# Performance work log

Hardware: AMD Instinct MI355X
Metric: run time of the kernel (lower is better)

The kernel has to match this reference:

```python
import jax, jax.numpy as jnp
import numpy as np

DIM, HEADS, DIM_HEAD, DY_DIM = 256, 8, 64, 16
INNER = HEADS * DIM_HEAD
B, N = 4, 1024
EPS = 1e-5


def _leaky(x):
    return jnp.where(x >= 0, x, 0.01 * x)


def _gelu(x):
    return jax.nn.gelu(x, approximate=False)  # torch nn.GELU default (erf)


def setup_inputs() -> dict:
    key = jax.random.key(0)
    ks = jax.random.split(key, 14)

    def lin(k, fan_in, fan_out):
        bound = 1.0 / np.sqrt(fan_in)
        return jax.random.uniform(k, (fan_in, fan_out), jnp.float32, -bound, bound)

    return {
        "xyzs": jax.random.normal(ks[0], (B, N, 3), jnp.float32),
        "features": jax.random.normal(ks[1], (B, N, DIM), jnp.float32),
        "gamma": jnp.ones((DIM,), jnp.float32),
        "beta": jnp.zeros((DIM,), jnp.float32),
        "W_qkv": lin(ks[2], DIM, 3 * INNER),
        "W_pos1": lin(ks[3], 3, DY_DIM),
        "W_pos2": lin(ks[4], DY_DIM, 3),
        "W_neg1": lin(ks[5], 3, DY_DIM),
        "W_neg2": lin(ks[6], DY_DIM, 3),
        "W_cross": lin(ks[7], 3, 3),
        "b_cross": jax.random.uniform(ks[8], (3,), jnp.float32, -0.5, 0.5),
        "W_spatial": lin(ks[9], 3, DIM_HEAD),
        "W_out": lin(ks[10], INNER, DIM),
        "b_out": jax.random.uniform(ks[11], (DIM,), jnp.float32, -1.0 / np.sqrt(INNER), 1.0 / np.sqrt(INNER)),
    }


def reference(xyzs, features, gamma, beta, W_qkv, W_pos1, W_pos2, W_neg1, W_neg2,
              W_cross, b_cross, W_spatial, W_out, b_out):
    b, n, dim = features.shape
    d = W_spatial.shape[1]                       # dim_head
    h = W_qkv.shape[1] // (3 * d)                # heads
    scale = d ** -0.5

    # LayerNorm
    mu = jnp.mean(features, axis=-1, keepdims=True)
    var = jnp.var(features, axis=-1, keepdims=True)
    x = (features - mu) * jax.lax.rsqrt(var + EPS) * gamma + beta

    # qkv projection -> (b, h, n, d)
    qkv = x @ W_qkv                              # (b, n, 3*h*d)
    q, k, v = jnp.split(qkv, 3, axis=-1)
    to_bhnd = lambda t: t.reshape(b, n, h, d).transpose(0, 2, 1, 3)
    q, k, v = to_bhnd(q), to_bhnd(k), to_bhnd(v)

    # pairwise deltas: delta[b, i, j] = xyzs[b, j] - xyzs[b, i]  (b, n, n, 3)
    delta = xyzs[:, None, :, :] - xyzs[:, :, None, :]

    pos = _leaky(_gelu(jax.nn.relu(delta) @ W_pos1) @ W_pos2)
    neg = _leaky(_gelu(jax.nn.relu(-delta) @ W_neg1) @ W_neg2)
    cross = _leaky((pos * neg) @ W_cross + b_cross)
    delta = cross * delta                        # (b, n, n, 3)

    # full softmax attention
    dots = jnp.einsum('bhid,bhjd->bhij', q, k) * scale
    attn = jax.nn.softmax(dots, axis=-1)         # (b, h, n, n)

    v_out = jnp.einsum('bhij,bhjd->bhid', attn, v)
    # attention-weighted reduction of pairwise deltas (no (b,h,n,n,3) materialization)
    wdelta = jnp.einsum('bhij,bijc->bhic', attn, delta)   # (b, h, n, 3)
    disp = wdelta @ W_spatial                    # (b, h, n, d)

    out = (v_out + disp).transpose(0, 2, 1, 3).reshape(b, n, h * d)
    out = _gelu(out @ W_out + b_out)             # to_out: Linear + GELU (dropout=0)
    return out + features
```

## Files before the change

### kernel.cpp

```cpp
#include <hip/hip_runtime.h>
#include <hip/hip_bf16.h>
#include <math.h>

#define BB 4
#define NN 1024
#define DIMM 256
#define HEADS 8
#define DH 64
#define INNERD 512
#define NT 16
#define MDPLANE 4194304

typedef __bf16 bf16x8 __attribute__((ext_vector_type(8)));
typedef float f32x4 __attribute__((ext_vector_type(4)));
typedef _Float16 h2 __attribute__((ext_vector_type(2)));

__device__ __forceinline__ h2 h2s(float v) {
    _Float16 h = (_Float16)v;
    h2 r; r.x = h; r.y = h;
    return r;
}

__device__ __forceinline__ float gelu_poly(float x) {
    float xc = fminf(fmaxf(x, -3.0f), 3.0f);
    float u = xc * xc;
    float f = fmaf(u, fmaf(u, fmaf(u, fmaf(u, 4.4413e-5f, -1.33195e-3f),
                                   1.70980e-2f), -1.299964e-1f), 7.9734583e-1f);
    float E = xc * f;
    float hx = 0.5f * xc;
    float g = fmaf(hx, E, hx);
    return g + fmaxf(x - 3.0f, 0.0f);
}

__device__ __forceinline__ h2 gelu_h2(h2 x) {
    h2 xc = __builtin_elementwise_min(__builtin_elementwise_max(x, h2s(-3.0f)), h2s(3.0f));
    h2 u = xc * xc;
    h2 f = u * h2s(2.22065e-5f) + h2s(-6.65975e-4f);
    f = u * f + h2s(8.549e-3f);
    f = u * f + h2s(-6.49982e-2f);
    f = u * f + h2s(0.39867292f);
    h2 g = xc * h2s(0.5f) + u * f;
    h2 tail = __builtin_elementwise_max(x - h2s(3.0f), h2s(0.0f));
    return g + tail;
}
__device__ __forceinline__ h2 leaky_h2(h2 x) {
    return __builtin_elementwise_max(x, x * h2s(0.01f));
}

__global__ __launch_bounds__(256) void prep_kernel(const float* __restrict__ feat,
                                                   const float* __restrict__ gamma,
                                                   const float* __restrict__ beta,
                                                   __hip_bfloat16* __restrict__ xb,
                                                   const float* __restrict__ Wqkv,
                                                   __hip_bfloat16* __restrict__ Wt,
                                                   const float* __restrict__ Wout,
                                                   __hip_bfloat16* __restrict__ Wot,
                                                   const float* __restrict__ Wp1,
                                                   const float* __restrict__ Wp2,
                                                   const float* __restrict__ Wn1,
                                                   const float* __restrict__ Wn2,
                                                   const float* __restrict__ Wc,
                                                   const float* __restrict__ bc,
                                                   unsigned int* __restrict__ wh) {
    __shared__ float smem[64 * 65];
    int bx = blockIdx.x;
    int tid = threadIdx.x;
    if (bx < 4096) {
        int row = bx;
        float v = feat[row * DIMM + tid];
        float s = v, ss = v * v;
        #pragma unroll
        for (int off = 1; off < 64; off <<= 1) {
            s += __shfl_xor(s, off);
            ss += __shfl_xor(ss, off);
        }
        float* red = smem;
        int w = tid >> 6, lane = tid & 63;
        if (lane == 0) { red[w] = s; red[4 + w] = ss; }
        __syncthreads();
        s = red[0] + red[1] + red[2] + red[3];
        ss = red[4] + red[5] + red[6] + red[7];
        float mu = s * (1.0f / DIMM);
        float var = ss * (1.0f / DIMM) - mu * mu;
        float rs = rsqrtf(var + 1e-5f);
        xb[row * DIMM + tid] = __float2bfloat16((v - mu) * rs * gamma[tid] + beta[tid]);
    } else if (bx < 4224) {
        const float* W;
        __hip_bfloat16* Wd;
        int C, R, nx, ky;
        if (bx < 4192) {
            int t = bx - 4096;
            W = Wqkv; Wd = Wt; C = 1536; R = 256;
            nx = t % 24; ky = t / 24;
        } else {
            int t = bx - 4192;
            W = Wout; Wd = Wot; C = 256; R = 512;
            nx = t % 4; ky = t / 4;
        }
        int n0 = nx * 64, k0 = ky * 64;
        int cc = tid & 63, rr = tid >> 6;
        #pragma unroll
        for (int p = 0; p < 16; ++p) {
            int k = rr + p * 4;
            smem[k * 65 + cc] = W[(k0 + k) * C + n0 + cc];
        }
        __syncthreads();
        #pragma unroll
        for (int p = 0; p < 16; ++p) {
            int n = rr + p * 4;
            Wd[(n0 + n) * R + k0 + cc] = __float2bfloat16(smem[cc * 65 + n]);
        }
    } else {
        int t = tid;
        if (t < 204) {
            float v;
            if (t < 48) v = Wp1[t];
            else if (t < 96) v = Wp2[t - 48];
            else if (t < 144) v = Wn1[t - 96];
            else if (t < 192) v = Wn2[t - 144];
            else if (t < 201) v = Wc[t - 192];
            else v = bc[t - 201];
            _Float16 h = (_Float16)v;
            unsigned short us = __builtin_bit_cast(unsigned short, h);
            wh[t] = (unsigned int)us | ((unsigned int)us << 16);
        }
    }
}

__device__ __forceinline__ void qkv_body(int bx,
                                         const __hip_bfloat16* __restrict__ xb,
                                         const __hip_bfloat16* __restrict__ Wt,
                                         __hip_bfloat16* __restrict__ qb,
                                         __hip_bfloat16* __restrict__ kb,
                                         __hip_bfloat16* __restrict__ vtb) {
    int mt = bx & 63, nt = bx >> 6;
    int tid = threadIdx.x, w = tid >> 6, lane = tid & 63;
    int g = lane >> 4, c = lane & 15;

    const __hip_bfloat16* ap = xb + (mt * 64 + w * 16 + c) * 256 + g * 8;
    bf16x8 a[8];
    #pragma unroll
    for (int ks = 0; ks < 8; ++ks) a[ks] = *reinterpret_cast<const bf16x8*>(ap + ks * 32);

    f32x4 acc[4];
    #pragma unroll
    for (int jf = 0; jf < 4; ++jf) { acc[jf][0] = 0.f; acc[jf][1] = 0.f; acc[jf][2] = 0.f; acc[jf][3] = 0.f; }

    const __hip_bfloat16* bp = Wt + (nt * 64 + c) * 256 + g * 8;
    #pragma unroll
    for (int jf = 0; jf < 4; ++jf) {
        const __hip_bfloat16* bpj = bp + jf * 16 * 256;
        #pragma unroll
        for (int ks = 0; ks < 8; ++ks) {
            bf16x8 bfrag = *reinterpret_cast<const bf16x8*>(bpj + ks * 32);
            acc[jf] = __builtin_amdgcn_mfma_f32_16x16x32_bf16(a[ks], bfrag, acc[jf], 0, 0, 0);
        }
    }

    int col0 = nt * 64;
    int part = col0 >> 9;
    int h = (col0 >> 6) & 7;
    #pragma unroll
    for (int jf = 0; jf < 4; ++jf) {
        int d = jf * 16 + c;
        #pragma unroll
        for (int r = 0; r < 4; ++r) {
            int m = mt * 64 + w * 16 + g * 4 + r;
            int b = m >> 10, nn = m & 1023;
            if (part == 0)
                qb[(((b * HEADS + h) * NN) + nn) * DH + d] = __float2bfloat16(acc[jf][r] * 0.125f);
            else if (part == 1)
                kb[(((b * HEADS + h) * NN) + nn) * DH + d] = __float2bfloat16(acc[jf][r]);
            else
                vtb[((long)(b * HEADS + h) * DH + d) * NN + nn] = __float2bfloat16(acc[jf][r]);
        }
    }
}

__device__ __forceinline__ void dmlp_body(int bx,
                                          const float* __restrict__ xyz,
                                          const unsigned int* __restrict__ wlds_u,
                                          _Float16* __restrict__ md) {
    int tid = threadIdx.x;
    int bi0 = bx * 4;
    int b = bi0 >> 10;
    const float* xj = xyz + (long)b * NN * 3;

    float xia[4], xib[4], xic[4];
    #pragma unroll
    for (int rr = 0; rr < 4; ++rr) {
        xia[rr] = xyz[(bi0 + rr) * 3 + 0];
        xib[rr] = xyz[(bi0 + rr) * 3 + 1];
        xic[rr] = xyz[(bi0 + rr) * 3 + 2];
    }

    const h2* w = (const h2*)wlds_u;

    h2 d0[8], d1[8], d2[8];
    #pragma unroll
    for (int g = 0; g < 2; ++g) {
        int j = 2 * tid + g * 512;
        const float* pj = xj + j * 3;
        float e0 = pj[0], e1 = pj[1], e2 = pj[2];
        float f0 = pj[3], f1 = pj[4], f2 = pj[5];
        #pragma unroll
        for (int rr = 0; rr < 4; ++rr) {
            int cg = rr * 2 + g;
            d0[cg].x = (_Float16)(e0 - xia[rr]); d0[cg].y = (_Float16)(f0 - xia[rr]);
            d1[cg].x = (_Float16)(e1 - xib[rr]); d1[cg].y = (_Float16)(f1 - xib[rr]);
            d2[cg].x = (_Float16)(e2 - xic[rr]); d2[cg].y = (_Float16)(f2 - xic[rr]);
        }
    }

    h2 pp0[8], pp1[8], pp2[8], nv0[8], nv1[8], nv2[8];
    {
        h2 r0[8], r1[8], r2[8], a0[8], a1[8], a2[8];
        #pragma unroll
        for (int cg = 0; cg < 8; ++cg) {
            r0[cg] = __builtin_elementwise_max(d0[cg], h2s(0.f));
            r1[cg] = __builtin_elementwise_max(d1[cg], h2s(0.f));
            r2[cg] = __builtin_elementwise_max(d2[cg], h2s(0.f));
            a0[cg] = h2s(0.f); a1[cg] = h2s(0.f); a2[cg] = h2s(0.f);
        }
        #pragma unroll
        for (int m = 0; m < 16; ++m) {
            h2 w0 = w[m], w1 = w[16 + m], w2 = w[32 + m];
            h2 u0 = w[48 + 3 * m], u1 = w[48 + 3 * m + 1], u2 = w[48 + 3 * m + 2];
            #pragma unroll
            for (int cg = 0; cg < 8; ++cg) {
                h2 t = r0[cg] * w0 + r1[cg] * w1 + r2[cg] * w2;
                t = gelu_h2(t);
                a0[cg] = a0[cg] + t * u0;
                a1[cg] = a1[cg] + t * u1;
                a2[cg] = a2[cg] + t * u2;
            }
        }
        #pragma unroll
        for (int cg = 0; cg < 8; ++cg) {
            pp0[cg] = leaky_h2(a0[cg]); pp1[cg] = leaky_h2(a1[cg]); pp2[cg] = leaky_h2(a2[cg]);
        }
    }
    {
        h2 r0[8], r1[8], r2[8], a0[8], a1[8], a2[8];
        #pragma unroll
        for (int cg = 0; cg < 8; ++cg) {
            r0[cg] = __builtin_elementwise_max(h2s(0.f) - d0[cg], h2s(0.f));
            r1[cg] = __builtin_elementwise_max(h2s(0.f) - d1[cg], h2s(0.f));
            r2[cg] = __builtin_elementwise_max(h2s(0.f) - d2[cg], h2s(0.f));
            a0[cg] = h2s(0.f); a1[cg] = h2s(0.f); a2[cg] = h2s(0.f);
        }
        #pragma unroll
        for (int m = 0; m < 16; ++m) {
            h2 w0 = w[96 + m], w1 = w[96 + 16 + m], w2 = w[96 + 32 + m];
            h2 u0 = w[144 + 3 * m], u1 = w[144 + 3 * m + 1], u2 = w[144 + 3 * m + 2];
            #pragma unroll
            for (int cg = 0; cg < 8; ++cg) {
                h2 t = r0[cg] * w0 + r1[cg] * w1 + r2[cg] * w2;
                t = gelu_h2(t);
                a0[cg] = a0[cg] + t * u0;
                a1[cg] = a1[cg] + t * u1;
                a2[cg] = a2[cg] + t * u2;
            }
        }
        #pragma unroll
        for (int cg = 0; cg < 8; ++cg) {
            nv0[cg] = leaky_h2(a0[cg]); nv1[cg] = leaky_h2(a1[cg]); nv2[cg] = leaky_h2(a2[cg]);
        }
    }

    h2 c00 = w[192], c01 = w[193], c02 = w[194];
    h2 c10 = w[195], c11 = w[196], c12 = w[197];
    h2 c20 = w[198], c21 = w[199], c22 = w[200];
    h2 b0 = w[201], b1 = w[202], b2 = w[203];

    unsigned int* st0 = (unsigned int*)md;
    unsigned int* st1 = (unsigned int*)(md + MDPLANE);
    unsigned int* st2 = (unsigned int*)(md + 2 * MDPLANE);
    #pragma unroll
    for (int rr = 0; rr < 4; ++rr) {
        long dwbase = (long)(bi0 + rr) * 512;
        #pragma unroll
        for (int g = 0; g < 2; ++g) {
            int cg = rr * 2 + g;
            h2 q0 = pp0[cg] * nv0[cg], q1 = pp1[cg] * nv1[cg], q2 = pp2[cg] * nv2[cg];
            h2 c0 = leaky_h2(q0 * c00 + q1 * c10 + q2 * c20 + b0);
            h2 c1 = leaky_h2(q0 * c01 + q1 * c11 + q2 * c21 + b1);
            h2 c2 = leaky_h2(q0 * c02 + q1 * c12 + q2 * c22 + b2);
            h2 m0 = c0 * d0[cg], m1 = c1 * d1[cg], m2 = c2 * d2[cg];
            long idx = dwbase + tid + g * 256;
            st0[idx] = __builtin_bit_cast(unsigned int, m0);
            st1[idx] = __builtin_bit_cast(unsigned int, m1);
            st2[idx] = __builtin_bit_cast(unsigned int, m2);
        }
    }
}

__global__ __launch_bounds__(256, 4) void fused_mid(const float* __restrict__ xyz,
                                                    const unsigned int* __restrict__ wh,
                                                    _Float16* __restrict__ md,
                                                    const __hip_bfloat16* __restrict__ xb,
                                                    const __hip_bfloat16* __restrict__ Wt,
                                                    __hip_bfloat16* __restrict__ qb,
                                                    __hip_bfloat16* __restrict__ kb,
                                                    __hip_bfloat16* __restrict__ vtb) {
    __shared__ unsigned int wlds[204];
    int bx = blockIdx.x;
    if (bx < 1024) {
        if (threadIdx.x < 204) wlds[threadIdx.x] = wh[threadIdx.x];
        __syncthreads();
        dmlp_body(bx, xyz, wlds, md);
    } else {
        qkv_body(bx - 1024, xb, Wt, qb, kb, vtb);
    }
}

__global__ __launch_bounds__(256) void attn_kernel(
    const __hip_bfloat16* __restrict__ q,
    const __hip_bfloat16* __restrict__ kk,
    const __hip_bfloat16* __restrict__ vt,
    const _Float16* __restrict__ md,
    const float* __restrict__ Wsp,
    __hip_bfloat16* __restrict__ yb)
{
    int it = blockIdx.x, h = blockIdx.y, b = blockIdx.z;
    int tid = threadIdx.x;
    int w = tid >> 6, lane = tid & 63;
    int g = lane >> 4, c = lane & 15;

    __shared__ __align__(16) __hip_bfloat16 k_lds[2][64][64];
    __shared__ __align__(16) __hip_bfloat16 v_lds[2][64][64];
    __shared__ __align__(16) __hip_bfloat16 p_lds[4][16][64];

    const __hip_bfloat16* qp = q + ((long)(b * HEADS + h) * NN + it * 64) * DH;
    const __hip_bfloat16* kp = kk + (long)(b * HEADS + h) * NN * DH;
    const __hip_bfloat16* vp = vt + (long)(b * HEADS + h) * DH * NN;

    bf16x8 qa[2];
    #pragma unroll
    for (int t2 = 0; t2 < 2; ++t2)
        qa[t2] = *reinterpret_cast<const bf16x8*>(qp + (w * 16 + c) * DH + t2 * 32 + g * 8);

    int r0 = tid >> 3;
    int d00 = (tid & 7) * 8;
    int4 kreg[2], vreg[2];

    f32x4 o[4];
    #pragma unroll
    for (int df = 0; df < 4; ++df) { o[df][0] = 0.f; o[df][1] = 0.f; o[df][2] = 0.f; o[df][3] = 0.f; }
    float m_[4] = {-1e30f, -1e30f, -1e30f, -1e30f};
    float l_[4] = {0.f, 0.f, 0.f, 0.f};
    float wdx[4] = {0.f, 0.f, 0.f, 0.f}, wdy[4] = {0.f, 0.f, 0.f, 0.f}, wdz[4] = {0.f, 0.f, 0.f, 0.f};

    #pragma unroll
    for (int c2 = 0; c2 < 2; ++c2) {
        int r = r0 + c2 * 32;
        kreg[c2] = *reinterpret_cast<const int4*>(kp + (0 * 64 + r) * DH + d00);
        vreg[c2] = *reinterpret_cast<const int4*>(vp + (long)r * NN + 0 * 64 + d00);
    }
    #pragma unroll
    for (int c2 = 0; c2 < 2; ++c2) {
        int r = r0 + c2 * 32;
        int sd = d00 ^ ((r & 7) << 3);
        *reinterpret_cast<int4*>(&k_lds[0][r][sd]) = kreg[c2];
        *reinterpret_cast<int4*>(&v_lds[0][r][sd]) = vreg[c2];
    }
    __syncthreads();

    const _Float16* md0 = md;
    const _Float16* md1 = md + MDPLANE;
    const _Float16* md2 = md + 2 * MDPLANE;
    long mdrow = (long)(b * NN + it * 64 + w * 16 + g * 4) * NN + c;

    for (int t = 0; t < NT; ++t) {
        int buf = t & 1;
        if (t + 1 < NT) {
            #pragma unroll
            for (int c2 = 0; c2 < 2; ++c2) {
                int r = r0 + c2 * 32;
                kreg[c2] = *reinterpret_cast<const int4*>(kp + ((t + 1) * 64 + r) * DH + d00);
                vreg[c2] = *reinterpret_cast<const int4*>(vp + (long)r * NN + (t + 1) * 64 + d00);
            }
        }

        float mdc[4][4][3];
        #pragma unroll
        for (int r = 0; r < 4; ++r) {
            long off = mdrow + (long)r * NN + t * 64;
            #pragma unroll
            for (int jf = 0; jf < 4; ++jf) {
                mdc[r][jf][0] = (float)md0[off + jf * 16];
                mdc[r][jf][1] = (float)md1[off + jf * 16];
                mdc[r][jf][2] = (float)md2[off + jf * 16];
            }
        }

        f32x4 s[4];
        #pragma unroll
        for (int jf = 0; jf < 4; ++jf) {
            f32x4 acc = {0.f, 0.f, 0.f, 0.f};
            int jl = jf * 16 + c;
            int sw = (jl & 7) << 3;
            #pragma unroll
            for (int t2 = 0; t2 < 2; ++t2) {
                bf16x8 bk = *reinterpret_cast<const bf16x8*>(&k_lds[buf][jl][(t2 * 32 + g * 8) ^ sw]);
                acc = __builtin_amdgcn_mfma_f32_16x16x32_bf16(qa[t2], bk, acc, 0, 0, 0);
            }
            s[jf] = acc;
        }

        float pe[4][4];
        #pragma unroll
        for (int r = 0; r < 4; ++r) {
            float tm = fmaxf(fmaxf(s[0][r], s[1][r]), fmaxf(s[2][r], s[3][r]));
            tm = fmaxf(tm, __shfl_xor(tm, 1));
            tm = fmaxf(tm, __shfl_xor(tm, 2));
            tm = fmaxf(tm, __shfl_xor(tm, 4));
            tm = fmaxf(tm, __shfl_xor(tm, 8));
            float nm = fmaxf(m_[r], tm);
            float corr = __expf(m_[r] - nm);
            m_[r] = nm;
            l_[r] *= corr;
            wdx[r] *= corr; wdy[r] *= corr; wdz[r] *= corr;
            o[0][r] *= corr; o[1][r] *= corr; o[2][r] *= corr; o[3][r] *= corr;
            float ps = 0.f;
            #pragma unroll
            for (int jf = 0; jf < 4; ++jf) {
                float p = __expf(s[jf][r] - nm);
                pe[r][jf] = p;
                ps += p;
            }
            l_[r] += ps;
        }

        #pragma unroll
        for (int r = 0; r < 4; ++r) {
            int row = g * 4 + r;
            int sw = (row & 7) << 3;
            #pragma unroll
            for (int jf = 0; jf < 4; ++jf)
                p_lds[w][row][(jf * 16 + c) ^ sw] = __float2bfloat16(pe[r][jf]);
        }
        asm volatile("s_waitcnt lgkmcnt(0)" ::: "memory");

        #pragma unroll
        for (int r = 0; r < 4; ++r) {
            #pragma unroll
            for (int jf = 0; jf < 4; ++jf) {
                wdx[r] = fmaf(pe[r][jf], mdc[r][jf][0], wdx[r]);
                wdy[r] = fmaf(pe[r][jf], mdc[r][jf][1], wdy[r]);
                wdz[r] = fmaf(pe[r][jf], mdc[r][jf][2], wdz[r]);
            }
        }

        #pragma unroll
        for (int t2 = 0; t2 < 2; ++t2) {
            int swp = (c & 7) << 3;
            bf16x8 pa = *reinterpret_cast<const bf16x8*>(&p_lds[w][c][(t2 * 32 + g * 8) ^ swp]);
            #pragma unroll
            for (int df = 0; df < 4; ++df) {
                int dl = df * 16 + c;
                int swv = (dl & 7) << 3;
                bf16x8 bv = *reinterpret_cast<const bf16x8*>(&v_lds[buf][dl][(t2 * 32 + g * 8) ^ swv]);
                o[df] = __builtin_amdgcn_mfma_f32_16x16x32_bf16(pa, bv, o[df], 0, 0, 0);
            }
        }

        if (t + 1 < NT) {
            #pragma unroll
            for (int c2 = 0; c2 < 2; ++c2) {
                int r = r0 + c2 * 32;
                int sd = d00 ^ ((r & 7) << 3);
                *reinterpret_cast<int4*>(&k_lds[buf ^ 1][r][sd]) = kreg[c2];
                *reinterpret_cast<int4*>(&v_lds[buf ^ 1][r][sd]) = vreg[c2];
            }
        }
        __syncthreads();
    }

    #pragma unroll
    for (int r = 0; r < 4; ++r) {
        float lv = l_[r];
        lv += __shfl_xor(lv, 1); lv += __shfl_xor(lv, 2);
        lv += __shfl_xor(lv, 4); lv += __shfl_xor(lv, 8);
        float w0 = wdx[r], w1 = wdy[r], w2 = wdz[r];
        w0 += __shfl_xor(w0, 1); w0 += __shfl_xor(w0, 2); w0 += __shfl_xor(w0, 4); w0 += __shfl_xor(w0, 8);
        w1 += __shfl_xor(w1, 1); w1 += __shfl_xor(w1, 2); w1 += __shfl_xor(w1, 4); w1 += __shfl_xor(w1, 8);
        w2 += __shfl_xor(w2, 1); w2 += __shfl_xor(w2, 2); w2 += __shfl_xor(w2, 4); w2 += __shfl_xor(w2, 8);
        float inv = 1.0f / lv;
        w0 *= inv; w1 *= inv; w2 *= inv;
        int row = g * 4 + r;
        long ig = (long)b * NN + it * 64 + w * 16 + row;
        __hip_bfloat16* yp = yb + ig * INNERD + h * DH;
        #pragma unroll
        for (int df = 0; df < 4; ++df) {
            int d = df * 16 + c;
            float disp = w0 * Wsp[d] + w1 * Wsp[64 + d] + w2 * Wsp[128 + d];
            yp[d] = __float2bfloat16(o[df][r] * inv + disp);
        }
    }
}

__global__ __launch_bounds__(256) void out_gemm(const __hip_bfloat16* __restrict__ yb,
                                                const __hip_bfloat16* __restrict__ Wot,
                                                const float* __restrict__ bout,
                                                const float* __restrict__ feat,
                                                float* __restrict__ out) {
    int mt = blockIdx.x, nt = blockIdx.y;
    int tid = threadIdx.x, w = tid >> 6, lane = tid & 63;
    int g = lane >> 4, c = lane & 15;

    const __hip_bfloat16* ap = yb + ((long)mt * 64 + w * 16 + c) * INNERD + g * 8;
    bf16x8 a[16];
    #pragma unroll
    for (int ks = 0; ks < 16; ++ks) a[ks] = *reinterpret_cast<const bf16x8*>(ap + ks * 32);

    f32x4 acc[4];
    #pragma unroll
    for (int jf = 0; jf < 4; ++jf) { acc[jf][0] = 0.f; acc[jf][1] = 0.f; acc[jf][2] = 0.f; acc[jf][3] = 0.f; }

    const __hip_bfloat16* bp = Wot + (nt * 64 + c) * INNERD + g * 8;
    #pragma unroll
    for (int jf = 0; jf < 4; ++jf) {
        const __hip_bfloat16* bpj = bp + jf * 16 * INNERD;
        #pragma unroll
        for (int ks = 0; ks < 16; ++ks) {
            bf16x8 bfrag = *reinterpret_cast<const bf16x8*>(bpj + ks * 32);
            acc[jf] = __builtin_amdgcn_mfma_f32_16x16x32_bf16(a[ks], bfrag, acc[jf], 0, 0, 0);
        }
    }

    #pragma unroll
    for (int jf = 0; jf < 4; ++jf) {
        int d = nt * 64 + jf * 16 + c;
        float bo = bout[d];
        #pragma unroll
        for (int r = 0; r < 4; ++r) {
            long m = (long)mt * 64 + w * 16 + g * 4 + r;
            float val = gelu_poly(acc[jf][r] + bo);
            out[m * DIMM + d] = val + feat[m * DIMM + d];
        }
    }
}

extern "C" void kernel_launch(void* const* d_in, const int* in_sizes, int n_in,
                              void* d_out, int out_size, void* d_ws, size_t ws_size,
                              hipStream_t stream) {
    const float* xyzs  = (const float*)d_in[0];
    const float* feat  = (const float*)d_in[1];
    const float* gamma = (const float*)d_in[2];
    const float* beta  = (const float*)d_in[3];
    const float* Wqkv  = (const float*)d_in[4];
    const float* Wp1   = (const float*)d_in[5];
    const float* Wp2   = (const float*)d_in[6];
    const float* Wn1   = (const float*)d_in[7];
    const float* Wn2   = (const float*)d_in[8];
    const float* Wc    = (const float*)d_in[9];
    const float* bc    = (const float*)d_in[10];
    const float* Wsp   = (const float*)d_in[11];
    const float* Wout  = (const float*)d_in[12];
    const float* bout  = (const float*)d_in[13];
    float* out = (float*)d_out;

    __hip_bfloat16* xb  = (__hip_bfloat16*)d_ws;
    __hip_bfloat16* Wt  = xb + 1048576;
    __hip_bfloat16* Wot = Wt + 393216;
    __hip_bfloat16* qb  = Wot + 131072;
    __hip_bfloat16* kb  = qb + 2097152;
    __hip_bfloat16* vtb = kb + 2097152;
    __hip_bfloat16* yb  = vtb + 2097152;
    _Float16* md = (_Float16*)(yb + 2097152);
    unsigned int* wh = (unsigned int*)(md + 3 * MDPLANE);

    prep_kernel<<<4225, 256, 0, stream>>>(feat, gamma, beta, xb, Wqkv, Wt, Wout, Wot,
                                          Wp1, Wp2, Wn1, Wn2, Wc, bc, wh);
    fused_mid<<<2560, 256, 0, stream>>>(xyzs, wh, md, xb, Wt, qb, kb, vtb);
    attn_kernel<<<dim3(16, HEADS, BB), 256, 0, stream>>>(qb, kb, vtb, md, Wsp, yb);
    out_gemm<<<dim3(64, 4), 256, 0, stream>>>(yb, Wot, bout, feat, out);
}
```

Baseline: 118.9 us.

## Split attention key range in two with a separate combine kernel

The attention grid doubles so each block processes half of the key tiles. Each block writes unnormalized partial outputs, its running max, its softmax sum and its weighted-delta sums to an fp32 workspace. A new combine kernel rescales and merges the two halves, applies the spatial projection and writes the bf16 activations. This raises the number of blocks available to fill the GPU, at the cost of extra global traffic for the partials and one more kernel launch.

```diff
diff --git a/kernel.cpp b/kernel.cpp
--- a/kernel.cpp
+++ b/kernel.cpp
@@ -10,6 +10,7 @@
 #define INNERD 512
 #define NT 16
 #define MDPLANE 4194304
+#define TOTROWS 32768
 
 typedef __bf16 bf16x8 __attribute__((ext_vector_type(8)));
 typedef float f32x4 __attribute__((ext_vector_type(4)));
@@ -319,10 +320,12 @@
     const __hip_bfloat16* __restrict__ kk,
     const __hip_bfloat16* __restrict__ vt,
     const _Float16* __restrict__ md,
-    const float* __restrict__ Wsp,
-    __hip_bfloat16* __restrict__ yb)
+    float* __restrict__ po,
+    float* __restrict__ pml)
 {
-    int it = blockIdx.x, h = blockIdx.y, b = blockIdx.z;
+    int it = blockIdx.x, h = blockIdx.y;
+    int z = blockIdx.z;
+    int b = z & 3, jh = z >> 2;
     int tid = threadIdx.x;
     int w = tid >> 6, lane = tid & 63;
     int g = lane >> 4, c = lane & 15;
@@ -351,11 +354,12 @@
     float l_[4] = {0.f, 0.f, 0.f, 0.f};
     float wdx[4] = {0.f, 0.f, 0.f, 0.f}, wdy[4] = {0.f, 0.f, 0.f, 0.f}, wdz[4] = {0.f, 0.f, 0.f, 0.f};
 
+    int t0 = jh * 8;
     #pragma unroll
     for (int c2 = 0; c2 < 2; ++c2) {
         int r = r0 + c2 * 32;
-        kreg[c2] = *reinterpret_cast<const int4*>(kp + (0 * 64 + r) * DH + d00);
-        vreg[c2] = *reinterpret_cast<const int4*>(vp + (long)r * NN + 0 * 64 + d00);
+        kreg[c2] = *reinterpret_cast<const int4*>(kp + (t0 * 64 + r) * DH + d00);
+        vreg[c2] = *reinterpret_cast<const int4*>(vp + (long)r * NN + t0 * 64 + d00);
     }
     #pragma unroll
     for (int c2 = 0; c2 < 2; ++c2) {
@@ -371,21 +375,22 @@
     const _Float16* md2 = md + 2 * MDPLANE;
     long mdrow = (long)(b * NN + it * 64 + w * 16 + g * 4) * NN + c;
 
-    for (int t = 0; t < NT; ++t) {
+    for (int t = 0; t < 8; ++t) {
+        int tt = t0 + t;
         int buf = t & 1;
-        if (t + 1 < NT) {
+        if (t + 1 < 8) {
             #pragma unroll
             for (int c2 = 0; c2 < 2; ++c2) {
                 int r = r0 + c2 * 32;
-                kreg[c2] = *reinterpret_cast<const int4*>(kp + ((t + 1) * 64 + r) * DH + d00);
-                vreg[c2] = *reinterpret_cast<const int4*>(vp + (long)r * NN + (t + 1) * 64 + d00);
+                kreg[c2] = *reinterpret_cast<const int4*>(kp + ((tt + 1) * 64 + r) * DH + d00);
+                vreg[c2] = *reinterpret_cast<const int4*>(vp + (long)r * NN + (tt + 1) * 64 + d00);
             }
         }
 
         float mdc[4][4][3];
         #pragma unroll
         for (int r = 0; r < 4; ++r) {
-            long off = mdrow + (long)r * NN + t * 64;
+            long off = mdrow + (long)r * NN + tt * 64;
             #pragma unroll
             for (int jf = 0; jf < 4; ++jf) {
                 mdc[r][jf][0] = (float)md0[off + jf * 16];
@@ -465,7 +470,7 @@
             }
         }
 
-        if (t + 1 < NT) {
+        if (t + 1 < 8) {
             #pragma unroll
             for (int c2 = 0; c2 < 2; ++c2) {
                 int r = r0 + c2 * 32;
@@ -486,18 +491,42 @@
         w0 += __shfl_xor(w0, 1); w0 += __shfl_xor(w0, 2); w0 += __shfl_xor(w0, 4); w0 += __shfl_xor(w0, 8);
         w1 += __shfl_xor(w1, 1); w1 += __shfl_xor(w1, 2); w1 += __shfl_xor(w1, 4); w1 += __shfl_xor(w1, 8);
         w2 += __shfl_xor(w2, 1); w2 += __shfl_xor(w2, 2); w2 += __shfl_xor(w2, 4); w2 += __shfl_xor(w2, 8);
-        float inv = 1.0f / lv;
-        w0 *= inv; w1 *= inv; w2 *= inv;
-        int row = g * 4 + r;
-        long ig = (long)b * NN + it * 64 + w * 16 + row;
-        __hip_bfloat16* yp = yb + ig * INNERD + h * DH;
-        #pragma unroll
-        for (int df = 0; df < 4; ++df) {
-            int d = df * 16 + c;
-            float disp = w0 * Wsp[d] + w1 * Wsp[64 + d] + w2 * Wsp[128 + d];
-            yp[d] = __float2bfloat16(o[df][r] * inv + disp);
-        }
-    }
+        int row = w * 16 + g * 4 + r;
+        long grow = (long)(b * HEADS + h) * NN + it * 64 + row;
+        float* pop = po + ((long)jh * TOTROWS + grow) * 64;
+        #pragma unroll
+        for (int df = 0; df < 4; ++df)
+            pop[df * 16 + c] = o[df][r];
+        if (c == 0) {
+            float* pm = pml + ((long)jh * TOTROWS + grow) * 8;
+            pm[0] = m_[r]; pm[1] = lv; pm[2] = w0; pm[3] = w1; pm[4] = w2;
+        }
+    }
+}
+
+__global__ __launch_bounds__(256) void combine_kernel(const float* __restrict__ po,
+                                                      const float* __restrict__ pml,
+                                                      const float* __restrict__ Wsp,
+                                                      __hip_bfloat16* __restrict__ yb) {
+    long row = (long)blockIdx.x * 4 + (threadIdx.x >> 6);
+    int d = threadIdx.x & 63;
+    const float* pm0 = pml + row * 8;
+    const float* pm1 = pml + ((long)TOTROWS + row) * 8;
+    float m0 = pm0[0], l0 = pm0[1];
+    float m1 = pm1[0], l1 = pm1[1];
+    float m = fmaxf(m0, m1);
+    float a0 = __expf(m0 - m), a1 = __expf(m1 - m);
+    float l = fmaf(l0, a0, l1 * a1);
+    float inv = 1.0f / l;
+    float ov = fmaf(po[row * 64 + d], a0, po[((long)TOTROWS + row) * 64 + d] * a1) * inv;
+    float wd0 = fmaf(pm0[2], a0, pm1[2] * a1) * inv;
+    float wd1 = fmaf(pm0[3], a0, pm1[3] * a1) * inv;
+    float wd2 = fmaf(pm0[4], a0, pm1[4] * a1) * inv;
+    float disp = wd0 * Wsp[d] + wd1 * Wsp[64 + d] + wd2 * Wsp[128 + d];
+    int b = (int)(row >> 13);
+    int h = (int)((row >> 10) & 7);
+    int i = (int)(row & 1023);
+    yb[((long)(b * NN + i)) * INNERD + h * DH + d] = __float2bfloat16(ov + disp);
 }
 
 __global__ __launch_bounds__(256) void out_gemm(const __hip_bfloat16* __restrict__ yb,
@@ -570,10 +599,13 @@
     __hip_bfloat16* yb  = vtb + 2097152;
     _Float16* md = (_Float16*)(yb + 2097152);
     unsigned int* wh = (unsigned int*)(md + 3 * MDPLANE);
+    float* po  = (float*)(wh + 256);
+    float* pml = po + 2L * TOTROWS * 64;
 
     prep_kernel<<<4225, 256, 0, stream>>>(feat, gamma, beta, xb, Wqkv, Wt, Wout, Wot,
                                           Wp1, Wp2, Wn1, Wn2, Wc, bc, wh);
     fused_mid<<<2560, 256, 0, stream>>>(xyzs, wh, md, xb, Wt, qb, kb, vtb);
-    attn_kernel<<<dim3(16, HEADS, BB), 256, 0, stream>>>(qb, kb, vtb, md, Wsp, yb);
+    attn_kernel<<<dim3(16, HEADS, BB * 2), 256, 0, stream>>>(qb, kb, vtb, md, po, pml);
+    combine_kernel<<<TOTROWS / 4, 256, 0, stream>>>(po, pml, Wsp, yb);
     out_gemm<<<dim3(64, 4), 256, 0, stream>>>(yb, Wot, bout, feat, out);
 }
```

Result: slower. 127.2 us (+6.9%).

## Regroup delta MLP with layernorm prep and split QKV GEMM into own kernel

Applied to the files above, without the earlier changes.

Moves the pairwise delta MLP work out of the QKV-GEMM kernel and into the first kernel alongside layernorm and weight transposes, converting the small MLP weights to fp16 in each block's shared memory instead of through a workspace buffer. The QKV GEMM becomes a standalone launch. The aim is to overlap the independent delta MLP with prep work rather than with the GEMM, and to drop the packed-weight round trip. It changes which work shares the GPU at once, which may help or hurt load balance.

```diff
diff --git a/kernel.cpp b/kernel.cpp
--- a/kernel.cpp
+++ b/kernel.cpp
@@ -45,136 +45,6 @@
 }
 __device__ __forceinline__ h2 leaky_h2(h2 x) {
     return __builtin_elementwise_max(x, x * h2s(0.01f));
-}
-
-__global__ __launch_bounds__(256) void prep_kernel(const float* __restrict__ feat,
-                                                   const float* __restrict__ gamma,
-                                                   const float* __restrict__ beta,
-                                                   __hip_bfloat16* __restrict__ xb,
-                                                   const float* __restrict__ Wqkv,
-                                                   __hip_bfloat16* __restrict__ Wt,
-                                                   const float* __restrict__ Wout,
-                                                   __hip_bfloat16* __restrict__ Wot,
-                                                   const float* __restrict__ Wp1,
-                                                   const float* __restrict__ Wp2,
-                                                   const float* __restrict__ Wn1,
-                                                   const float* __restrict__ Wn2,
-                                                   const float* __restrict__ Wc,
-                                                   const float* __restrict__ bc,
-                                                   unsigned int* __restrict__ wh) {
-    __shared__ float smem[64 * 65];
-    int bx = blockIdx.x;
-    int tid = threadIdx.x;
-    if (bx < 4096) {
-        int row = bx;
-        float v = feat[row * DIMM + tid];
-        float s = v, ss = v * v;
-        #pragma unroll
-        for (int off = 1; off < 64; off <<= 1) {
-            s += __shfl_xor(s, off);
-            ss += __shfl_xor(ss, off);
-        }
-        float* red = smem;
-        int w = tid >> 6, lane = tid & 63;
-        if (lane == 0) { red[w] = s; red[4 + w] = ss; }
-        __syncthreads();
-        s = red[0] + red[1] + red[2] + red[3];
-        ss = red[4] + red[5] + red[6] + red[7];
-        float mu = s * (1.0f / DIMM);
-        float var = ss * (1.0f / DIMM) - mu * mu;
-        float rs = rsqrtf(var + 1e-5f);
-        xb[row * DIMM + tid] = __float2bfloat16((v - mu) * rs * gamma[tid] + beta[tid]);
-    } else if (bx < 4224) {
-        const float* W;
-        __hip_bfloat16* Wd;
-        int C, R, nx, ky;
-        if (bx < 4192) {
-            int t = bx - 4096;
-            W = Wqkv; Wd = Wt; C = 1536; R = 256;
-            nx = t % 24; ky = t / 24;
-        } else {
-            int t = bx - 4192;
-            W = Wout; Wd = Wot; C = 256; R = 512;
-            nx = t % 4; ky = t / 4;
-        }
-        int n0 = nx * 64, k0 = ky * 64;
-        int cc = tid & 63, rr = tid >> 6;
-        #pragma unroll
-        for (int p = 0; p < 16; ++p) {
-            int k = rr + p * 4;
-            smem[k * 65 + cc] = W[(k0 + k) * C + n0 + cc];
-        }
-        __syncthreads();
-        #pragma unroll
-        for (int p = 0; p < 16; ++p) {
-            int n = rr + p * 4;
-            Wd[(n0 + n) * R + k0 + cc] = __float2bfloat16(smem[cc * 65 + n]);
-        }
-    } else {
-        int t = tid;
-        if (t < 204) {
-            float v;
-            if (t < 48) v = Wp1[t];
-            else if (t < 96) v = Wp2[t - 48];
-            else if (t < 144) v = Wn1[t - 96];
-            else if (t < 192) v = Wn2[t - 144];
-            else if (t < 201) v = Wc[t - 192];
-            else v = bc[t - 201];
-            _Float16 h = (_Float16)v;
-            unsigned short us = __builtin_bit_cast(unsigned short, h);
-            wh[t] = (unsigned int)us | ((unsigned int)us << 16);
-        }
-    }
-}
-
-__device__ __forceinline__ void qkv_body(int bx,
-                                         const __hip_bfloat16* __restrict__ xb,
-                                         const __hip_bfloat16* __restrict__ Wt,
-                                         __hip_bfloat16* __restrict__ qb,
-                                         __hip_bfloat16* __restrict__ kb,
-                                         __hip_bfloat16* __restrict__ vtb) {
-    int mt = bx & 63, nt = bx >> 6;
-    int tid = threadIdx.x, w = tid >> 6, lane = tid & 63;
-    int g = lane >> 4, c = lane & 15;
-
-    const __hip_bfloat16* ap = xb + (mt * 64 + w * 16 + c) * 256 + g * 8;
-    bf16x8 a[8];
-    #pragma unroll
-    for (int ks = 0; ks < 8; ++ks) a[ks] = *reinterpret_cast<const bf16x8*>(ap + ks * 32);
-
-    f32x4 acc[4];
-    #pragma unroll
-    for (int jf = 0; jf < 4; ++jf) { acc[jf][0] = 0.f; acc[jf][1] = 0.f; acc[jf][2] = 0.f; acc[jf][3] = 0.f; }
-
-    const __hip_bfloat16* bp = Wt + (nt * 64 + c) * 256 + g * 8;
-    #pragma unroll
-    for (int jf = 0; jf < 4; ++jf) {
-        const __hip_bfloat16* bpj = bp + jf * 16 * 256;
-        #pragma unroll
-        for (int ks = 0; ks < 8; ++ks) {
-            bf16x8 bfrag = *reinterpret_cast<const bf16x8*>(bpj + ks * 32);
-            acc[jf] = __builtin_amdgcn_mfma_f32_16x16x32_bf16(a[ks], bfrag, acc[jf], 0, 0, 0);
-        }
-    }
-
-    int col0 = nt * 64;
-    int part = col0 >> 9;
-    int h = (col0 >> 6) & 7;
-    #pragma unroll
-    for (int jf = 0; jf < 4; ++jf) {
-        int d = jf * 16 + c;
-        #pragma unroll
-        for (int r = 0; r < 4; ++r) {
-            int m = mt * 64 + w * 16 + g * 4 + r;
-            int b = m >> 10, nn = m & 1023;
-            if (part == 0)
-                qb[(((b * HEADS + h) * NN) + nn) * DH + d] = __float2bfloat16(acc[jf][r] * 0.125f);
-            else if (part == 1)
-                kb[(((b * HEADS + h) * NN) + nn) * DH + d] = __float2bfloat16(acc[jf][r]);
-            else
-                vtb[((long)(b * HEADS + h) * DH + d) * NN + nn] = __float2bfloat16(acc[jf][r]);
-        }
-    }
 }
 
 __device__ __forceinline__ void dmlp_body(int bx,
@@ -295,22 +165,136 @@
     }
 }
 
-__global__ __launch_bounds__(256, 4) void fused_mid(const float* __restrict__ xyz,
-                                                    const unsigned int* __restrict__ wh,
-                                                    _Float16* __restrict__ md,
-                                                    const __hip_bfloat16* __restrict__ xb,
-                                                    const __hip_bfloat16* __restrict__ Wt,
-                                                    __hip_bfloat16* __restrict__ qb,
-                                                    __hip_bfloat16* __restrict__ kb,
-                                                    __hip_bfloat16* __restrict__ vtb) {
-    __shared__ unsigned int wlds[204];
+__global__ __launch_bounds__(256, 4) void pre_mid(const float* __restrict__ xyz,
+                                                  const float* __restrict__ Wp1,
+                                                  const float* __restrict__ Wp2,
+                                                  const float* __restrict__ Wn1,
+                                                  const float* __restrict__ Wn2,
+                                                  const float* __restrict__ Wc,
+                                                  const float* __restrict__ bc,
+                                                  _Float16* __restrict__ md,
+                                                  const float* __restrict__ feat,
+                                                  const float* __restrict__ gamma,
+                                                  const float* __restrict__ beta,
+                                                  __hip_bfloat16* __restrict__ xb,
+                                                  const float* __restrict__ Wqkv,
+                                                  __hip_bfloat16* __restrict__ Wt,
+                                                  const float* __restrict__ Wout,
+                                                  __hip_bfloat16* __restrict__ Wot) {
+    __shared__ float smem[64 * 65];
     int bx = blockIdx.x;
+    int tid = threadIdx.x;
     if (bx < 1024) {
-        if (threadIdx.x < 204) wlds[threadIdx.x] = wh[threadIdx.x];
+        unsigned int* wlds = (unsigned int*)smem;
+        if (tid < 204) {
+            float v;
+            if (tid < 48) v = Wp1[tid];
+            else if (tid < 96) v = Wp2[tid - 48];
+            else if (tid < 144) v = Wn1[tid - 96];
+            else if (tid < 192) v = Wn2[tid - 144];
+            else if (tid < 201) v = Wc[tid - 192];
+            else v = bc[tid - 201];
+            _Float16 h = (_Float16)v;
+            unsigned short us = __builtin_bit_cast(unsigned short, h);
+            wlds[tid] = (unsigned int)us | ((unsigned int)us << 16);
+        }
         __syncthreads();
         dmlp_body(bx, xyz, wlds, md);
+    } else if (bx < 5120) {
+        int row = bx - 1024;
+        float v = feat[row * DIMM + tid];
+        float s = v, ss = v * v;
+        #pragma unroll
+        for (int off = 1; off < 64; off <<= 1) {
+            s += __shfl_xor(s, off);
+            ss += __shfl_xor(ss, off);
+        }
+        float* red = smem;
+        int w = tid >> 6, lane = tid & 63;
+        if (lane == 0) { red[w] = s; red[4 + w] = ss; }
+        __syncthreads();
+        s = red[0] + red[1] + red[2] + red[3];
+        ss = red[4] + red[5] + red[6] + red[7];
+        float mu = s * (1.0f / DIMM);
+        float var = ss * (1.0f / DIMM) - mu * mu;
+        float rs = rsqrtf(var + 1e-5f);
+        xb[row * DIMM + tid] = __float2bfloat16((v - mu) * rs * gamma[tid] + beta[tid]);
     } else {
-        qkv_body(bx - 1024, xb, Wt, qb, kb, vtb);
+        const float* W;
+        __hip_bfloat16* Wd;
+        int C, R, nx, ky;
+        int t = bx - 5120;
+        if (t < 96) {
+            W = Wqkv; Wd = Wt; C = 1536; R = 256;
+            nx = t % 24; ky = t / 24;
+        } else {
+            t -= 96;
+            W = Wout; Wd = Wot; C = 256; R = 512;
+            nx = t % 4; ky = t / 4;
+        }
+        int n0 = nx * 64, k0 = ky * 64;
+        int cc = tid & 63, rr = tid >> 6;
+        #pragma unroll
+        for (int p = 0; p < 16; ++p) {
+            int k = rr + p * 4;
+            smem[k * 65 + cc] = W[(k0 + k) * C + n0 + cc];
+        }
+        __syncthreads();
+        #pragma unroll
+        for (int p = 0; p < 16; ++p) {
+            int n = rr + p * 4;
+            Wd[(n0 + n) * R + k0 + cc] = __float2bfloat16(smem[cc * 65 + n]);
+        }
+    }
+}
+
+__global__ __launch_bounds__(256) void qkv_gemm(const __hip_bfloat16* __restrict__ xb,
+                                                const __hip_bfloat16* __restrict__ Wt,
+                                                __hip_bfloat16* __restrict__ qb,
+                                                __hip_bfloat16* __restrict__ kb,
+                                                __hip_bfloat16* __restrict__ vtb) {
+    int bx = blockIdx.x;
+    int mt = bx & 63, nt = bx >> 6;
+    int tid = threadIdx.x, w = tid >> 6, lane = tid & 63;
+    int g = lane >> 4, c = lane & 15;
+
+    const __hip_bfloat16* ap = xb + (mt * 64 + w * 16 + c) * 256 + g * 8;
+    bf16x8 a[8];
+    #pragma unroll
+    for (int ks = 0; ks < 8; ++ks) a[ks] = *reinterpret_cast<const bf16x8*>(ap + ks * 32);
+
+    f32x4 acc[4];
+    #pragma unroll
+    for (int jf = 0; jf < 4; ++jf) { acc[jf][0] = 0.f; acc[jf][1] = 0.f; acc[jf][2] = 0.f; acc[jf][3] = 0.f; }
+
+    const __hip_bfloat16* bp = Wt + (nt * 64 + c) * 256 + g * 8;
+    #pragma unroll
+    for (int jf = 0; jf < 4; ++jf) {
+        const __hip_bfloat16* bpj = bp + jf * 16 * 256;
+        #pragma unroll
+        for (int ks = 0; ks < 8; ++ks) {
+            bf16x8 bfrag = *reinterpret_cast<const bf16x8*>(bpj + ks * 32);
+            acc[jf] = __builtin_amdgcn_mfma_f32_16x16x32_bf16(a[ks], bfrag, acc[jf], 0, 0, 0);
+        }
+    }
+
+    int col0 = nt * 64;
+    int part = col0 >> 9;
+    int h = (col0 >> 6) & 7;
+    #pragma unroll
+    for (int jf = 0; jf < 4; ++jf) {
+        int d = jf * 16 + c;
+        #pragma unroll
+        for (int r = 0; r < 4; ++r) {
+            int m = mt * 64 + w * 16 + g * 4 + r;
+            int b = m >> 10, nn = m & 1023;
+            if (part == 0)
+                qb[(((b * HEADS + h) * NN) + nn) * DH + d] = __float2bfloat16(acc[jf][r] * 0.125f);
+            else if (part == 1)
+                kb[(((b * HEADS + h) * NN) + nn) * DH + d] = __float2bfloat16(acc[jf][r]);
+            else
+                vtb[((long)(b * HEADS + h) * DH + d) * NN + nn] = __float2bfloat16(acc[jf][r]);
+        }
     }
 }
 
@@ -569,11 +553,10 @@
     __hip_bfloat16* vtb = kb + 2097152;
     __hip_bfloat16* yb  = vtb + 2097152;
     _Float16* md = (_Float16*)(yb + 2097152);
-    unsigned int* wh = (unsigned int*)(md + 3 * MDPLANE);
-
-    prep_kernel<<<4225, 256, 0, stream>>>(feat, gamma, beta, xb, Wqkv, Wt, Wout, Wot,
-                                          Wp1, Wp2, Wn1, Wn2, Wc, bc, wh);
-    fused_mid<<<2560, 256, 0, stream>>>(xyzs, wh, md, xb, Wt, qb, kb, vtb);
+
+    pre_mid<<<5248, 256, 0, stream>>>(xyzs, Wp1, Wp2, Wn1, Wn2, Wc, bc, md,
+                                      feat, gamma, beta, xb, Wqkv, Wt, Wout, Wot);
+    qkv_gemm<<<1536, 256, 0, stream>>>(xb, Wt, qb, kb, vtb);
     attn_kernel<<<dim3(16, HEADS, BB), 256, 0, stream>>>(qb, kb, vtb, md, Wsp, yb);
     out_gemm<<<dim3(64, 4), 256, 0, stream>>>(yb, Wot, bout, feat, out);
 }
```

Result: slower. 132.6 us (+11.5%).
